# Kernel optimization log

Hardware: AMD Instinct MI355X
Metric: run time of the kernel (lower is better)

## Reference

```python
import jax, jax.numpy as jnp
import numpy as np

SEQ, BATCH, HIDDEN = 4096, 16, 512

def setup_inputs() -> dict:
    key = jax.random.key(0)
    kf, kx, kh = jax.random.split(key, 3)
    f = jax.random.uniform(kf, (SEQ, BATCH, HIDDEN), dtype=jnp.float32)
    x = jax.random.normal(kx, (SEQ, BATCH, HIDDEN), dtype=jnp.float32)
    hidden_init = jax.random.normal(kh, (BATCH, HIDDEN), dtype=jnp.float32)
    return {"f": f, "x": x, "hidden_init": hidden_init}

def reference(f, x, hidden_init):
    # h_t = f_t * x_t + (1 - f_t) * h_{t-1}
    # Linear recurrence h_t = a_t * h_{t-1} + b_t with a = 1-f, b = f*x.
    # Solved with an associative scan: compose (a1,b1) then (a2,b2) ->
    # (a1*a2, a2*b1 + b2). After the scan, A_t = prod(a_1..a_t) and
    # B_t = h_t assuming h_0 = 0, so h_t = B_t + A_t * h_init.
    a = 1.0 - f                      # (S, B, H)
    b = f * x                        # (S, B, H)

    def combine(c1, c2):
        a1, b1 = c1
        a2, b2 = c2
        return (a1 * a2, a2 * b1 + b2)

    A, B = jax.lax.associative_scan(combine, (a, b), axis=0)
    return B + A * hidden_init[None, :, :]
```

## Files before the change

kernel.cpp:

```cpp
#include <hip/hip_runtime.h>


#define SQ      4096
#define NC4     2048
#define NCH     8192
#define TT      32
#define NCHUNK  (SQ / TT)
#define CB      8
#define GRID1   (NCHUNK * CB)

typedef float floatx4 __attribute__((ext_vector_type(4)));

__global__ __launch_bounds__(256, 4)
void fm_agg(const float4* __restrict__ f4, const float4* __restrict__ x4,
            float4* __restrict__ aggA, float4* __restrict__ aggB)
{
  const int tid   = threadIdx.x;
  const int chunk = blockIdx.x >> 3;
  const int col   = ((blockIdx.x & 7) << 8) + tid;
  const size_t base = (size_t)(chunk * TT) * NC4 + col;

  float ax = 1.f, ay = 1.f, az = 1.f, aw = 1.f;
  float bx = 0.f, by = 0.f, bz = 0.f, bw = 0.f;

  for (int batch = 0; batch < TT / 8; ++batch) {
    float4 ff[8], xx[8];
#pragma unroll
    for (int i = 0; i < 8; ++i) {
      const size_t idx = base + (size_t)(batch * 8 + i) * NC4;
      ff[i] = f4[idx];
      xx[i] = x4[idx];
    }
#pragma unroll
    for (int i = 0; i < 8; ++i) {
      bx = fmaf(ff[i].x, xx[i].x - bx, bx);
      by = fmaf(ff[i].y, xx[i].y - by, by);
      bz = fmaf(ff[i].z, xx[i].z - bz, bz);
      bw = fmaf(ff[i].w, xx[i].w - bw, bw);
      ax = fmaf(-ff[i].x, ax, ax);
      ay = fmaf(-ff[i].y, ay, ay);
      az = fmaf(-ff[i].z, az, az);
      aw = fmaf(-ff[i].w, aw, aw);
    }
  }
  float4 A; A.x = ax; A.y = ay; A.z = az; A.w = aw;
  float4 B; B.x = bx; B.y = by; B.z = bz; B.w = bw;
  aggA[(size_t)chunk * NC4 + col] = A;
  aggB[(size_t)chunk * NC4 + col] = B;
}

__global__ __launch_bounds__(256, 4)
void fm_mid(const float* __restrict__ A, const float* __restrict__ B,
            const float* __restrict__ h0, float* __restrict__ hprev)
{
  const int chain = blockIdx.x * 256 + threadIdx.x;
  float h = h0[chain];
  for (int cb = 0; cb < NCHUNK / 16; ++cb) {
    float a[16], b[16];
#pragma unroll
    for (int i = 0; i < 16; ++i) {
      const size_t idx = (size_t)(cb * 16 + i) * NCH + chain;
      a[i] = A[idx];
      b[i] = B[idx];
    }
#pragma unroll
    for (int i = 0; i < 16; ++i) {
      const size_t idx = (size_t)(cb * 16 + i) * NCH + chain;
      hprev[idx] = h;
      h = fmaf(a[i], h, b[i]);
    }
  }
}

__global__ __launch_bounds__(256, 4)
void fm_apply(const float4* __restrict__ f4, const float4* __restrict__ x4,
              const float4* __restrict__ hprev4, float4* __restrict__ out4)
{
  const int tid   = threadIdx.x;
  const int chunk = (NCHUNK - 1) - (blockIdx.x >> 3);
  const int col   = ((blockIdx.x & 7) << 8) + tid;
  const size_t base = (size_t)(chunk * TT) * NC4 + col;

  floatx4* __restrict__ outv = (floatx4*)out4;

  float4 h = hprev4[(size_t)chunk * NC4 + col];
  for (int batch = 0; batch < TT / 8; ++batch) {
    float4 ff[8], xx[8];
#pragma unroll
    for (int i = 0; i < 8; ++i) {
      const size_t idx = base + (size_t)(batch * 8 + i) * NC4;
      ff[i] = f4[idx];
      xx[i] = x4[idx];
    }
#pragma unroll
    for (int i = 0; i < 8; ++i) {
      h.x = fmaf(ff[i].x, xx[i].x - h.x, h.x);
      h.y = fmaf(ff[i].y, xx[i].y - h.y, h.y);
      h.z = fmaf(ff[i].z, xx[i].z - h.z, h.z);
      h.w = fmaf(ff[i].w, xx[i].w - h.w, h.w);
      floatx4 hv; hv.x = h.x; hv.y = h.y; hv.z = h.z; hv.w = h.w;
      __builtin_nontemporal_store(hv, &outv[base + (size_t)(batch * 8 + i) * NC4]);
    }
  }
}

__global__ void fm_naive(const float4* __restrict__ f4, const float4* __restrict__ x4,
                         const float4* __restrict__ h04, float4* __restrict__ out4)
{
  const int col = blockIdx.x * blockDim.x + threadIdx.x;
  if (col >= NC4) return;
  float4 h = h04[col];
  for (int t = 0; t < SQ; ++t) {
    const size_t idx = (size_t)t * NC4 + col;
    const float4 ff = f4[idx], xx = x4[idx];
    h.x = fmaf(ff.x, xx.x - h.x, h.x);
    h.y = fmaf(ff.y, xx.y - h.y, h.y);
    h.z = fmaf(ff.z, xx.z - h.z, h.z);
    h.w = fmaf(ff.w, xx.w - h.w, h.w);
    out4[idx] = h;
  }
}

extern "C" void kernel_launch(void* const* d_in, const int* in_sizes, int n_in,
                              void* d_out, int out_size, void* d_ws, size_t ws_size,
                              hipStream_t stream)
{
  const float4* f4  = (const float4*)d_in[0];
  const float4* x4  = (const float4*)d_in[1];
  const float4* h04 = (const float4*)d_in[2];
  float4* out4 = (float4*)d_out;

  const size_t AGG = (size_t)NCHUNK * NC4 * 16;
  const size_t HPV = (size_t)NCHUNK * NCH * 4;
  const size_t need = 2 * AGG + HPV;

  if (ws_size >= need) {
    float4* aggA   = (float4*)d_ws;
    float4* aggB   = (float4*)((char*)d_ws + AGG);
    float*  hprev  = (float*)((char*)d_ws + 2 * AGG);
    fm_agg<<<GRID1, 256, 0, stream>>>(f4, x4, aggA, aggB);
    fm_mid<<<NCH / 256, 256, 0, stream>>>((const float*)aggA, (const float*)aggB,
                                          (const float*)h04, hprev);
    fm_apply<<<GRID1, 256, 0, stream>>>(f4, x4, (const float4*)hprev, out4);
  } else {
    fm_naive<<<(NC4 + 255) / 256, 256, 0, stream>>>(f4, x4, h04, out4);
  }
}
```

Baseline: 369.9 us.

## Shrink chunk length, widen blocks to full rows, prefetch, reuse B buffer for hprev

Chunk length drops from 32 to 16 timesteps and each 512-thread block now covers a whole row of 2048 float4 columns, four per thread. Loads are double-buffered one timestep ahead. The mid pass writes carry-in states in place over the B aggregate, which removes the separate hprev buffer. The apply pass no longer walks chunks in reverse order. The shorter chunks double the aggregate traffic and the sequential length of the mid pass, and launch_bounds(512,1) may limit occupancy.

```diff
diff --git a/kernel.cpp b/kernel.cpp
--- a/kernel.cpp
+++ b/kernel.cpp
@@ -4,54 +4,68 @@
 #define SQ      4096
 #define NC4     2048
 #define NCH     8192
-#define TT      32
+#define TT      16
 #define NCHUNK  (SQ / TT)
-#define CB      8
-#define GRID1   (NCHUNK * CB)
 
 typedef float floatx4 __attribute__((ext_vector_type(4)));
 
-__global__ __launch_bounds__(256, 4)
+__global__ __launch_bounds__(512, 1)
 void fm_agg(const float4* __restrict__ f4, const float4* __restrict__ x4,
             float4* __restrict__ aggA, float4* __restrict__ aggB)
 {
   const int tid   = threadIdx.x;
-  const int chunk = blockIdx.x >> 3;
-  const int col   = ((blockIdx.x & 7) << 8) + tid;
-  const size_t base = (size_t)(chunk * TT) * NC4 + col;
+  const int chunk = blockIdx.x;
+  const size_t rowbase = (size_t)chunk * TT * NC4 + tid;
 
-  float ax = 1.f, ay = 1.f, az = 1.f, aw = 1.f;
-  float bx = 0.f, by = 0.f, bz = 0.f, bw = 0.f;
+  float4 A[4], B[4];
+#pragma unroll
+  for (int j = 0; j < 4; ++j) {
+    A[j].x = 1.f; A[j].y = 1.f; A[j].z = 1.f; A[j].w = 1.f;
+    B[j].x = 0.f; B[j].y = 0.f; B[j].z = 0.f; B[j].w = 0.f;
+  }
 
-  for (int batch = 0; batch < TT / 8; ++batch) {
-    float4 ff[8], xx[8];
+  float4 ff[2][4], xx[2][4];
 #pragma unroll
-    for (int i = 0; i < 8; ++i) {
-      const size_t idx = base + (size_t)(batch * 8 + i) * NC4;
-      ff[i] = f4[idx];
-      xx[i] = x4[idx];
+  for (int j = 0; j < 4; ++j) {
+    ff[0][j] = f4[rowbase + 512 * j];
+    xx[0][j] = x4[rowbase + 512 * j];
+  }
+
+#pragma unroll
+  for (int t = 0; t < TT; ++t) {
+    const int cur = t & 1, nxt = cur ^ 1;
+    if (t + 1 < TT) {
+      const size_t r = rowbase + (size_t)(t + 1) * NC4;
+#pragma unroll
+      for (int j = 0; j < 4; ++j) {
+        ff[nxt][j] = f4[r + 512 * j];
+        xx[nxt][j] = x4[r + 512 * j];
+      }
     }
 #pragma unroll
-    for (int i = 0; i < 8; ++i) {
-      bx = fmaf(ff[i].x, xx[i].x - bx, bx);
-      by = fmaf(ff[i].y, xx[i].y - by, by);
-      bz = fmaf(ff[i].z, xx[i].z - bz, bz);
-      bw = fmaf(ff[i].w, xx[i].w - bw, bw);
-      ax = fmaf(-ff[i].x, ax, ax);
-      ay = fmaf(-ff[i].y, ay, ay);
-      az = fmaf(-ff[i].z, az, az);
-      aw = fmaf(-ff[i].w, aw, aw);
+    for (int j = 0; j < 4; ++j) {
+      const float4 f_ = ff[cur][j], x_ = xx[cur][j];
+      B[j].x = fmaf(f_.x, x_.x - B[j].x, B[j].x);
+      B[j].y = fmaf(f_.y, x_.y - B[j].y, B[j].y);
+      B[j].z = fmaf(f_.z, x_.z - B[j].z, B[j].z);
+      B[j].w = fmaf(f_.w, x_.w - B[j].w, B[j].w);
+      A[j].x = fmaf(-f_.x, A[j].x, A[j].x);
+      A[j].y = fmaf(-f_.y, A[j].y, A[j].y);
+      A[j].z = fmaf(-f_.z, A[j].z, A[j].z);
+      A[j].w = fmaf(-f_.w, A[j].w, A[j].w);
     }
   }
-  float4 A; A.x = ax; A.y = ay; A.z = az; A.w = aw;
-  float4 B; B.x = bx; B.y = by; B.z = bz; B.w = bw;
-  aggA[(size_t)chunk * NC4 + col] = A;
-  aggB[(size_t)chunk * NC4 + col] = B;
+
+#pragma unroll
+  for (int j = 0; j < 4; ++j) {
+    aggA[(size_t)chunk * NC4 + tid + 512 * j] = A[j];
+    aggB[(size_t)chunk * NC4 + tid + 512 * j] = B[j];
+  }
 }
 
 __global__ __launch_bounds__(256, 4)
-void fm_mid(const float* __restrict__ A, const float* __restrict__ B,
-            const float* __restrict__ h0, float* __restrict__ hprev)
+void fm_mid(const float* __restrict__ A, float* __restrict__ B,
+            const float* __restrict__ h0)
 {
   const int chain = blockIdx.x * 256 + threadIdx.x;
   float h = h0[chain];
@@ -66,40 +80,54 @@
 #pragma unroll
     for (int i = 0; i < 16; ++i) {
       const size_t idx = (size_t)(cb * 16 + i) * NCH + chain;
-      hprev[idx] = h;
+      B[idx] = h;
       h = fmaf(a[i], h, b[i]);
     }
   }
 }
 
-__global__ __launch_bounds__(256, 4)
+__global__ __launch_bounds__(512, 1)
 void fm_apply(const float4* __restrict__ f4, const float4* __restrict__ x4,
               const float4* __restrict__ hprev4, float4* __restrict__ out4)
 {
   const int tid   = threadIdx.x;
-  const int chunk = (NCHUNK - 1) - (blockIdx.x >> 3);
-  const int col   = ((blockIdx.x & 7) << 8) + tid;
-  const size_t base = (size_t)(chunk * TT) * NC4 + col;
-
+  const int chunk = blockIdx.x;
+  const size_t rowbase = (size_t)chunk * TT * NC4 + tid;
   floatx4* __restrict__ outv = (floatx4*)out4;
 
-  float4 h = hprev4[(size_t)chunk * NC4 + col];
-  for (int batch = 0; batch < TT / 8; ++batch) {
-    float4 ff[8], xx[8];
+  float4 h[4];
 #pragma unroll
-    for (int i = 0; i < 8; ++i) {
-      const size_t idx = base + (size_t)(batch * 8 + i) * NC4;
-      ff[i] = f4[idx];
-      xx[i] = x4[idx];
+  for (int j = 0; j < 4; ++j)
+    h[j] = hprev4[(size_t)chunk * NC4 + tid + 512 * j];
+
+  float4 ff[2][4], xx[2][4];
+#pragma unroll
+  for (int j = 0; j < 4; ++j) {
+    ff[0][j] = f4[rowbase + 512 * j];
+    xx[0][j] = x4[rowbase + 512 * j];
+  }
+
+#pragma unroll
+  for (int t = 0; t < TT; ++t) {
+    const int cur = t & 1, nxt = cur ^ 1;
+    if (t + 1 < TT) {
+      const size_t r = rowbase + (size_t)(t + 1) * NC4;
+#pragma unroll
+      for (int j = 0; j < 4; ++j) {
+        ff[nxt][j] = f4[r + 512 * j];
+        xx[nxt][j] = x4[r + 512 * j];
+      }
     }
+    const size_t ro = rowbase + (size_t)t * NC4;
 #pragma unroll
-    for (int i = 0; i < 8; ++i) {
-      h.x = fmaf(ff[i].x, xx[i].x - h.x, h.x);
-      h.y = fmaf(ff[i].y, xx[i].y - h.y, h.y);
-      h.z = fmaf(ff[i].z, xx[i].z - h.z, h.z);
-      h.w = fmaf(ff[i].w, xx[i].w - h.w, h.w);
-      floatx4 hv; hv.x = h.x; hv.y = h.y; hv.z = h.z; hv.w = h.w;
-      __builtin_nontemporal_store(hv, &outv[base + (size_t)(batch * 8 + i) * NC4]);
+    for (int j = 0; j < 4; ++j) {
+      const float4 f_ = ff[cur][j], x_ = xx[cur][j];
+      h[j].x = fmaf(f_.x, x_.x - h[j].x, h[j].x);
+      h[j].y = fmaf(f_.y, x_.y - h[j].y, h[j].y);
+      h[j].z = fmaf(f_.z, x_.z - h[j].z, h[j].z);
+      h[j].w = fmaf(f_.w, x_.w - h[j].w, h[j].w);
+      floatx4 hv; hv.x = h[j].x; hv.y = h[j].y; hv.z = h[j].z; hv.w = h[j].w;
+      __builtin_nontemporal_store(hv, &outv[ro + 512 * j]);
     }
   }
 }
@@ -131,17 +159,14 @@
   float4* out4 = (float4*)d_out;
 
   const size_t AGG = (size_t)NCHUNK * NC4 * 16;
-  const size_t HPV = (size_t)NCHUNK * NCH * 4;
-  const size_t need = 2 * AGG + HPV;
 
-  if (ws_size >= need) {
-    float4* aggA   = (float4*)d_ws;
-    float4* aggB   = (float4*)((char*)d_ws + AGG);
-    float*  hprev  = (float*)((char*)d_ws + 2 * AGG);
-    fm_agg<<<GRID1, 256, 0, stream>>>(f4, x4, aggA, aggB);
-    fm_mid<<<NCH / 256, 256, 0, stream>>>((const float*)aggA, (const float*)aggB,
-                                          (const float*)h04, hprev);
-    fm_apply<<<GRID1, 256, 0, stream>>>(f4, x4, (const float4*)hprev, out4);
+  if (ws_size >= 2 * AGG) {
+    float4* aggA = (float4*)d_ws;
+    float4* aggB = (float4*)((char*)d_ws + AGG);
+    fm_agg<<<NCHUNK, 512, 0, stream>>>(f4, x4, aggA, aggB);
+    fm_mid<<<NCH / 256, 256, 0, stream>>>((const float*)aggA,
+                                          (float*)aggB, (const float*)h04);
+    fm_apply<<<NCHUNK, 512, 0, stream>>>(f4, x4, (const float4*)aggB, out4);
   } else {
     fm_naive<<<(NC4 + 255) / 256, 256, 0, stream>>>(f4, x4, h04, out4);
   }
```

After: 369.6 us. No clear change (-0.1%).

## Halve scan chunk length, preload whole chunk, and reuse aggB for carry-in

Applied to the files above, without the earlier changes.

Chunk length drops from 32 to 16 timesteps, which doubles the number of chunks and the grid size of the aggregate and apply kernels. Each thread now issues all 16 chunk loads up front, with a scheduling barrier that keeps them ahead of the serial FMA chain, and launch bounds are relaxed to allow more registers. The middle kernel overwrites aggB in place with the carry-in states instead of writing a separate hprev buffer, which cuts workspace size and one buffer's traffic. In exchange, the middle serial scan runs twice as many steps per chain and the aggregate arrays double in size.

```diff
diff --git a/kernel.cpp b/kernel.cpp
--- a/kernel.cpp
+++ b/kernel.cpp
@@ -4,54 +4,49 @@
 #define SQ      4096
 #define NC4     2048
 #define NCH     8192
-#define TT      32
+#define TT      16
 #define NCHUNK  (SQ / TT)
-#define CB      8
-#define GRID1   (NCHUNK * CB)
+#define GRID1   (NCHUNK * 8)
 
 typedef float floatx4 __attribute__((ext_vector_type(4)));
 
-__global__ __launch_bounds__(256, 4)
-void fm_agg(const float4* __restrict__ f4, const float4* __restrict__ x4,
-            float4* __restrict__ aggA, float4* __restrict__ aggB)
+__global__ __launch_bounds__(256, 2)
+void fm_agg(const floatx4* __restrict__ f4, const floatx4* __restrict__ x4,
+            floatx4* __restrict__ aggA, floatx4* __restrict__ aggB)
 {
   const int tid   = threadIdx.x;
   const int chunk = blockIdx.x >> 3;
   const int col   = ((blockIdx.x & 7) << 8) + tid;
   const size_t base = (size_t)(chunk * TT) * NC4 + col;
 
-  float ax = 1.f, ay = 1.f, az = 1.f, aw = 1.f;
-  float bx = 0.f, by = 0.f, bz = 0.f, bw = 0.f;
+  floatx4 ff[TT], xx[TT];
+#pragma unroll
+  for (int t = 0; t < TT; ++t) {
+    ff[t] = f4[base + (size_t)t * NC4];
+    xx[t] = x4[base + (size_t)t * NC4];
+  }
+  __builtin_amdgcn_sched_barrier(0);
 
-  for (int batch = 0; batch < TT / 8; ++batch) {
-    float4 ff[8], xx[8];
+  floatx4 A = {1.f, 1.f, 1.f, 1.f};
+  floatx4 B = {0.f, 0.f, 0.f, 0.f};
 #pragma unroll
-    for (int i = 0; i < 8; ++i) {
-      const size_t idx = base + (size_t)(batch * 8 + i) * NC4;
-      ff[i] = f4[idx];
-      xx[i] = x4[idx];
-    }
-#pragma unroll
-    for (int i = 0; i < 8; ++i) {
-      bx = fmaf(ff[i].x, xx[i].x - bx, bx);
-      by = fmaf(ff[i].y, xx[i].y - by, by);
-      bz = fmaf(ff[i].z, xx[i].z - bz, bz);
-      bw = fmaf(ff[i].w, xx[i].w - bw, bw);
-      ax = fmaf(-ff[i].x, ax, ax);
-      ay = fmaf(-ff[i].y, ay, ay);
-      az = fmaf(-ff[i].z, az, az);
-      aw = fmaf(-ff[i].w, aw, aw);
-    }
+  for (int t = 0; t < TT; ++t) {
+    B.x = fmaf(ff[t].x, xx[t].x - B.x, B.x);
+    B.y = fmaf(ff[t].y, xx[t].y - B.y, B.y);
+    B.z = fmaf(ff[t].z, xx[t].z - B.z, B.z);
+    B.w = fmaf(ff[t].w, xx[t].w - B.w, B.w);
+    A.x = fmaf(-ff[t].x, A.x, A.x);
+    A.y = fmaf(-ff[t].y, A.y, A.y);
+    A.z = fmaf(-ff[t].z, A.z, A.z);
+    A.w = fmaf(-ff[t].w, A.w, A.w);
   }
-  float4 A; A.x = ax; A.y = ay; A.z = az; A.w = aw;
-  float4 B; B.x = bx; B.y = by; B.z = bz; B.w = bw;
   aggA[(size_t)chunk * NC4 + col] = A;
   aggB[(size_t)chunk * NC4 + col] = B;
 }
 
 __global__ __launch_bounds__(256, 4)
-void fm_mid(const float* __restrict__ A, const float* __restrict__ B,
-            const float* __restrict__ h0, float* __restrict__ hprev)
+void fm_mid(const float* __restrict__ A, float* __restrict__ B,
+            const float* __restrict__ h0)
 {
   const int chain = blockIdx.x * 256 + threadIdx.x;
   float h = h0[chain];
@@ -66,41 +61,37 @@
 #pragma unroll
     for (int i = 0; i < 16; ++i) {
       const size_t idx = (size_t)(cb * 16 + i) * NCH + chain;
-      hprev[idx] = h;
+      B[idx] = h;
       h = fmaf(a[i], h, b[i]);
     }
   }
 }
 
-__global__ __launch_bounds__(256, 4)
-void fm_apply(const float4* __restrict__ f4, const float4* __restrict__ x4,
-              const float4* __restrict__ hprev4, float4* __restrict__ out4)
+__global__ __launch_bounds__(256, 2)
+void fm_apply(const floatx4* __restrict__ f4, const floatx4* __restrict__ x4,
+              const floatx4* __restrict__ hprev4, floatx4* __restrict__ out4)
 {
   const int tid   = threadIdx.x;
   const int chunk = (NCHUNK - 1) - (blockIdx.x >> 3);
   const int col   = ((blockIdx.x & 7) << 8) + tid;
   const size_t base = (size_t)(chunk * TT) * NC4 + col;
 
-  floatx4* __restrict__ outv = (floatx4*)out4;
+  floatx4 ff[TT], xx[TT];
+#pragma unroll
+  for (int t = 0; t < TT; ++t) {
+    ff[t] = f4[base + (size_t)t * NC4];
+    xx[t] = x4[base + (size_t)t * NC4];
+  }
+  floatx4 h = hprev4[(size_t)chunk * NC4 + col];
+  __builtin_amdgcn_sched_barrier(0);
 
-  float4 h = hprev4[(size_t)chunk * NC4 + col];
-  for (int batch = 0; batch < TT / 8; ++batch) {
-    float4 ff[8], xx[8];
 #pragma unroll
-    for (int i = 0; i < 8; ++i) {
-      const size_t idx = base + (size_t)(batch * 8 + i) * NC4;
-      ff[i] = f4[idx];
-      xx[i] = x4[idx];
-    }
-#pragma unroll
-    for (int i = 0; i < 8; ++i) {
-      h.x = fmaf(ff[i].x, xx[i].x - h.x, h.x);
-      h.y = fmaf(ff[i].y, xx[i].y - h.y, h.y);
-      h.z = fmaf(ff[i].z, xx[i].z - h.z, h.z);
-      h.w = fmaf(ff[i].w, xx[i].w - h.w, h.w);
-      floatx4 hv; hv.x = h.x; hv.y = h.y; hv.z = h.z; hv.w = h.w;
-      __builtin_nontemporal_store(hv, &outv[base + (size_t)(batch * 8 + i) * NC4]);
-    }
+  for (int t = 0; t < TT; ++t) {
+    h.x = fmaf(ff[t].x, xx[t].x - h.x, h.x);
+    h.y = fmaf(ff[t].y, xx[t].y - h.y, h.y);
+    h.z = fmaf(ff[t].z, xx[t].z - h.z, h.z);
+    h.w = fmaf(ff[t].w, xx[t].w - h.w, h.w);
+    __builtin_nontemporal_store(h, &out4[base + (size_t)t * NC4]);
   }
 }
 
@@ -125,24 +116,24 @@
                               void* d_out, int out_size, void* d_ws, size_t ws_size,
                               hipStream_t stream)
 {
-  const float4* f4  = (const float4*)d_in[0];
-  const float4* x4  = (const float4*)d_in[1];
-  const float4* h04 = (const float4*)d_in[2];
-  float4* out4 = (float4*)d_out;
+  const floatx4* f4  = (const floatx4*)d_in[0];
+  const floatx4* x4  = (const floatx4*)d_in[1];
+  const float*   h0  = (const float*)d_in[2];
+  floatx4* out4 = (floatx4*)d_out;
 
   const size_t AGG = (size_t)NCHUNK * NC4 * 16;
-  const size_t HPV = (size_t)NCHUNK * NCH * 4;
-  const size_t need = 2 * AGG + HPV;
 
-  if (ws_size >= need) {
-    float4* aggA   = (float4*)d_ws;
-    float4* aggB   = (float4*)((char*)d_ws + AGG);
-    float*  hprev  = (float*)((char*)d_ws + 2 * AGG);
+  if (ws_size >= 2 * AGG) {
+    floatx4* aggA = (floatx4*)d_ws;
+    floatx4* aggB = (floatx4*)((char*)d_ws + AGG);
     fm_agg<<<GRID1, 256, 0, stream>>>(f4, x4, aggA, aggB);
-    fm_mid<<<NCH / 256, 256, 0, stream>>>((const float*)aggA, (const float*)aggB,
-                                          (const float*)h04, hprev);
-    fm_apply<<<GRID1, 256, 0, stream>>>(f4, x4, (const float4*)hprev, out4);
+    fm_mid<<<NCH / 256, 256, 0, stream>>>((const float*)aggA,
+                                          (float*)aggB, h0);
+    fm_apply<<<GRID1, 256, 0, stream>>>(f4, x4, (const floatx4*)aggB, out4);
   } else {
-    fm_naive<<<(NC4 + 255) / 256, 256, 0, stream>>>(f4, x4, h04, out4);
+    fm_naive<<<(NC4 + 255) / 256, 256, 0, stream>>>((const float4*)f4,
+                                                    (const float4*)x4,
+                                                    (const float4*)h0,
+                                                    (float4*)out4);
   }
 }
```

New measurement: 371.0 us. Within noise of the previous version (+0.3%).
